# Optimization experiments

Measured on AMD Instinct MI355X. Metric: run time of the kernel, lower is better.

Reference implementation:

```python
import jax, jax.numpy as jnp
import numpy as np

L, D, DFF, H, B, S = 6, 1024, 4096, 16, 4, 512
DK = D // H
EPS = 1e-6


def setup_inputs() -> dict:
    key = jax.random.key(0)
    ks = jax.random.split(key, 20)
    sc = 0.02
    n = jax.random.normal
    return {
        "x": n(ks[0], (B, S, D), jnp.float32),
        "Wq": n(ks[1], (L, D, D)) * sc, "bq": jnp.zeros((L, D)),
        "Wk": n(ks[2], (L, D, D)) * sc, "bk": jnp.zeros((L, D)),
        "Wv": n(ks[3], (L, D, D)) * sc, "bv": jnp.zeros((L, D)),
        "Wo": n(ks[4], (L, D, D)) * sc, "bo": jnp.zeros((L, D)),
        "W1": n(ks[5], (L, D, DFF)) * sc, "b1": jnp.zeros((L, DFF)),
        "W2": n(ks[6], (L, DFF, D)) * sc, "b2": jnp.zeros((L, D)),
        "ln1_a": jnp.ones((L, D)), "ln1_b": jnp.zeros((L, D)),
        "ln2_a": jnp.ones((L, D)), "ln2_b": jnp.zeros((L, D)),
        "norm_a": jnp.ones((D,)), "norm_b": jnp.zeros((D,)),
    }


def _ln(x, a, b):
    # custom LayerNorm: uses sample std (ddof=1, like torch.std) and (std + eps)
    m = x.mean(-1, keepdims=True)
    s = jnp.std(x, axis=-1, ddof=1, keepdims=True)
    return a * (x - m) / (s + EPS) + b


def reference(x, Wq, bq, Wk, bk, Wv, bv, Wo, bo, W1, b1, W2, b2,
              ln1_a, ln1_b, ln2_a, ln2_b, norm_a, norm_b):
    inv = 1.0 / jnp.sqrt(jnp.float32(DK))
    for l in range(L):
        # --- self-attention sublayer (pre-norm, residual) ---
        h = _ln(x, ln1_a[l], ln1_b[l])
        q = (h @ Wq[l] + bq[l]).reshape(B, S, H, DK)
        k = (h @ Wk[l] + bk[l]).reshape(B, S, H, DK)
        v = (h @ Wv[l] + bv[l]).reshape(B, S, H, DK)
        scores = jnp.einsum('bqhd,bkhd->bhqk', q, k) * inv
        p = jax.nn.softmax(scores, axis=-1)
        o = jnp.einsum('bhqk,bkhd->bqhd', p, v).reshape(B, S, D)
        x = x + (o @ Wo[l] + bo[l])
        # --- feed-forward sublayer ---
        h = _ln(x, ln2_a[l], ln2_b[l])
        x = x + (jax.nn.relu(h @ W1[l] + b1[l]) @ W2[l] + b2[l])
    return _ln(x, norm_a, norm_b)
```

## Files before the change

### kernel.cpp

```cpp
#include <hip/hip_runtime.h>
#include <hip/hip_bf16.h>

typedef __hip_bfloat16 bf16;
typedef __bf16 bf16x8 __attribute__((ext_vector_type(8)));
typedef float f32x4 __attribute__((ext_vector_type(4)));

static constexpr int L_ = 6, D_ = 1024, DFF_ = 4096, H_ = 16, B_ = 4, S_ = 512, DK_ = 64;
static constexpr int N_ = B_ * S_;

#define GLOAD_LDS(gp, lp) __builtin_amdgcn_global_load_lds( \
    (const __attribute__((address_space(1))) void*)(gp),    \
    (__attribute__((address_space(3))) void*)(lp), 16, 0, 0)

__global__ void transpose_cast(const float* __restrict__ in, bf16* __restrict__ out,
                               int K, int M, long zin, long zout) {
    const float* ip = in + (size_t)blockIdx.z * zin;
    bf16* op = out + (size_t)blockIdx.z * zout;
    __shared__ float t[32][33];
    int m0 = blockIdx.x * 32, k0 = blockIdx.y * 32;
    int tx = threadIdx.x, ty = threadIdx.y;
    #pragma unroll
    for (int i = 0; i < 32; i += 8)
        t[ty + i][tx] = ip[(size_t)(k0 + ty + i) * M + m0 + tx];
    __syncthreads();
    #pragma unroll
    for (int i = 0; i < 32; i += 8)
        op[(size_t)(m0 + ty + i) * K + k0 + tx] = __float2bfloat16(t[tx][ty + i]);
}

__global__ void pack_qkv_bias(const float* __restrict__ bq, const float* __restrict__ bk,
                              const float* __restrict__ bv, float* __restrict__ out) {
    int t = blockIdx.x * 256 + threadIdx.x;
    int l = t / (3 * D_), c = t % (3 * D_);
    float v = c < D_ ? bq[l * D_ + c] : (c < 2 * D_ ? bk[l * D_ + c - D_] : bv[l * D_ + c - 2 * D_]);
    out[t] = v;
}

template <typename OutT>
__global__ __launch_bounds__(256) void ln_kernel(const float* __restrict__ x,
                                                 const float* __restrict__ ga,
                                                 const float* __restrict__ gb,
                                                 OutT* __restrict__ out) {
    int row = blockIdx.x;
    float4 v = ((const float4*)(x + (size_t)row * D_))[threadIdx.x];
    float s = v.x + v.y + v.z + v.w;
    float q = v.x * v.x + v.y * v.y + v.z * v.z + v.w * v.w;
    #pragma unroll
    for (int m = 1; m < 64; m <<= 1) { s += __shfl_xor(s, m, 64); q += __shfl_xor(q, m, 64); }
    __shared__ float ps[4], pq[4];
    int wid = threadIdx.x >> 6;
    if ((threadIdx.x & 63) == 0) { ps[wid] = s; pq[wid] = q; }
    __syncthreads();
    s = ps[0] + ps[1] + ps[2] + ps[3];
    q = pq[0] + pq[1] + pq[2] + pq[3];
    float mean = s * (1.0f / D_);
    float var = (q - (float)D_ * mean * mean) * (1.0f / (D_ - 1));
    var = var < 0.f ? 0.f : var;
    float rstd = 1.0f / (sqrtf(var) + 1e-6f);
    int c = threadIdx.x * 4;
    float xv[4] = {v.x, v.y, v.z, v.w};
    #pragma unroll
    for (int r = 0; r < 4; r++) {
        float o = ga[c + r] * (xv[r] - mean) * rstd + gb[c + r];
        if constexpr (__hip_internal::is_same<OutT, float>::value)
            out[(size_t)row * D_ + c + r] = o;
        else
            out[(size_t)row * D_ + c + r] = __float2bfloat16(o);
    }
}

template <int S, typename OutT>
__global__ __launch_bounds__(256) void reduce_ln(
    const bf16* __restrict__ parts, long sK, float* __restrict__ xf,
    const float* __restrict__ ga, const float* __restrict__ gb, OutT* __restrict__ out) {
    int row = blockIdx.x;
    float4 v = ((const float4*)(xf + (size_t)row * D_))[threadIdx.x];
    #pragma unroll
    for (int s = 0; s < S; s++) {
        ushort4 u = ((const ushort4*)(parts + (size_t)s * sK + (size_t)row * D_))[threadIdx.x];
        v.x += __uint_as_float((unsigned)u.x << 16);
        v.y += __uint_as_float((unsigned)u.y << 16);
        v.z += __uint_as_float((unsigned)u.z << 16);
        v.w += __uint_as_float((unsigned)u.w << 16);
    }
    ((float4*)(xf + (size_t)row * D_))[threadIdx.x] = v;
    float sum = v.x + v.y + v.z + v.w;
    float q = v.x * v.x + v.y * v.y + v.z * v.z + v.w * v.w;
    #pragma unroll
    for (int m = 1; m < 64; m <<= 1) { sum += __shfl_xor(sum, m, 64); q += __shfl_xor(q, m, 64); }
    __shared__ float ps[4], pq[4];
    int wid = threadIdx.x >> 6;
    if ((threadIdx.x & 63) == 0) { ps[wid] = sum; pq[wid] = q; }
    __syncthreads();
    sum = ps[0] + ps[1] + ps[2] + ps[3];
    q = pq[0] + pq[1] + pq[2] + pq[3];
    float mean = sum * (1.0f / D_);
    float var = (q - (float)D_ * mean * mean) * (1.0f / (D_ - 1));
    var = var < 0.f ? 0.f : var;
    float rstd = 1.0f / (sqrtf(var) + 1e-6f);
    int c = threadIdx.x * 4;
    float xv[4] = {v.x, v.y, v.z, v.w};
    #pragma unroll
    for (int r = 0; r < 4; r++) {
        float o = ga[c + r] * (xv[r] - mean) * rstd + gb[c + r];
        if constexpr (__hip_internal::is_same<OutT, float>::value)
            out[(size_t)row * D_ + c + r] = o;
        else
            out[(size_t)row * D_ + c + r] = __float2bfloat16(o);
    }
}

__device__ inline void swz_tiles(int& ntile, int& mtile) {
    unsigned o = blockIdx.y * gridDim.x + blockIdx.x;
    if ((gridDim.x & 7) == 0) {
        unsigned xcd = o & 7, j = o >> 3;
        unsigned cn = gridDim.x >> 3;
        ntile = xcd * cn + j / gridDim.y;
        mtile = j % gridDim.y;
    } else {
        ntile = o % gridDim.x;
        mtile = o / gridDim.x;
    }
}

enum { EPI_RELU = 0, EPI_PART = 1, EPI_QKV = 2 };

template <int EPI, int SPLITK = 1>
__global__ __launch_bounds__(256) void gemm4(
    const bf16* __restrict__ A, int lda,
    const bf16* __restrict__ Bt, int ldb,
    const float* __restrict__ bias,
    void* __restrict__ Cv, int ldc, long sK, int K,
    bf16* __restrict__ qb, bf16* __restrict__ kb, bf16* __restrict__ vT) {
    constexpr int BM = 128, BN = 64, BK = 64;
    constexpr int FM = 4, FN = 2;
    constexpr int IA = 4;
    constexpr int IB = 2;
    __shared__ __align__(16) bf16 As[BM * BK];
    __shared__ __align__(16) bf16 Bs[BN * BK];
    const int tid = threadIdx.x, wid = tid >> 6, lane = tid & 63;
    const int kz = (SPLITK > 1) ? blockIdx.z : 0;
    int ntile, mtile;
    swz_tiles(ntile, mtile);
    const int m0 = mtile * BM, n0 = ntile * BN;
    const int wm = (wid >> 1) * 64, wn = (wid & 1) * 32;
    const int fr = lane & 15, fg = lane >> 4;
    const int sr = lane >> 3;
    const int c8s = (lane & 7) ^ (sr & 7);
    const int Kc = K / SPLITK;
    const int kbeg = kz * Kc, kend = kbeg + Kc;

    f32x4 acc[FM][FN] = {};
    for (int k0 = kbeg; k0 < kend; k0 += BK) {
        __syncthreads();
        #pragma unroll
        for (int i = 0; i < IA; i++) {
            int inst = wid * IA + i;
            const bf16* gp = A + (size_t)(m0 + inst * 8 + sr) * lda + k0 + c8s * 8;
            GLOAD_LDS(gp, &As[inst * 512]);
        }
        #pragma unroll
        for (int i = 0; i < IB; i++) {
            int inst = wid * IB + i;
            const bf16* gp = Bt + (size_t)(n0 + inst * 8 + sr) * ldb + k0 + c8s * 8;
            GLOAD_LDS(gp, &Bs[inst * 512]);
        }
        __syncthreads();
        #pragma unroll
        for (int kk = 0; kk < 2; kk++) {
            const int cs = ((kk << 2) + fg) ^ (fr & 7);
            bf16x8 af[FM], bfr[FN];
            #pragma unroll
            for (int i = 0; i < FM; i++)
                af[i] = *(const bf16x8*)&As[(wm + i * 16 + fr) * BK + cs * 8];
            #pragma unroll
            for (int j = 0; j < FN; j++)
                bfr[j] = *(const bf16x8*)&Bs[(wn + j * 16 + fr) * BK + cs * 8];
            #pragma unroll
            for (int i = 0; i < FM; i++)
                #pragma unroll
                for (int j = 0; j < FN; j++)
                    acc[i][j] = __builtin_amdgcn_mfma_f32_16x16x32_bf16(af[i], bfr[j], acc[i][j], 0, 0, 0);
        }
    }
    #pragma unroll
    for (int i = 0; i < FM; i++) {
        #pragma unroll
        for (int j = 0; j < FN; j++) {
            int rr = m0 + wm + i * 16 + (lane >> 4) * 4;
            int cc = n0 + wn + j * 16 + (lane & 15);
            float bv = bias[cc];
            #pragma unroll
            for (int r = 0; r < 4; r++) {
                float v = acc[i][j][r];
                if constexpr (EPI == EPI_RELU) {
                    bf16* C = (bf16*)Cv;
                    float o = v + bv;
                    C[(size_t)(rr + r) * ldc + cc] = __float2bfloat16(o > 0.f ? o : 0.f);
                } else if constexpr (EPI == EPI_PART) {
                    bf16* C = (bf16*)Cv;
                    C[(size_t)kz * sK + (size_t)(rr + r) * ldc + cc] =
                        __float2bfloat16(v + (kz == 0 ? bv : 0.f));
                } else {
                    float o = v + bv;
                    if (cc < D_) {
                        qb[(size_t)(rr + r) * D_ + cc] = __float2bfloat16(o);
                    } else if (cc < 2 * D_) {
                        kb[(size_t)(rr + r) * D_ + cc - D_] = __float2bfloat16(o);
                    } else {
                        vT[((size_t)(rr >> 9) * D_ + cc - 2 * D_) * S_ + ((rr & 511) + r)] = __float2bfloat16(o);
                    }
                }
            }
        }
    }
}

__global__ __launch_bounds__(256) void flash_attn(
    const bf16* __restrict__ qb, const bf16* __restrict__ kb, const bf16* __restrict__ vT,
    bf16* __restrict__ ob) {
    __shared__ __align__(16) bf16 P[4][16 * 64];
    const int lane = threadIdx.x & 63, wid = threadIdx.x >> 6;
    const int b = blockIdx.y >> 4, h = blockIdx.y & 15;
    const int q0 = blockIdx.x * 64 + wid * 16;
    const int fr = lane & 15, fg = lane >> 4;
    bf16* Pw = &P[wid][0];

    const bf16* qrow = qb + ((size_t)(b * S_ + q0 + fr)) * D_ + h * DK_ + fg * 8;
    bf16x8 aq0 = *(const bf16x8*)(qrow);
    bf16x8 aq1 = *(const bf16x8*)(qrow + 32);
    const bf16* vbase = vT + ((size_t)(b * D_) + h * DK_ + fr) * S_ + fg * 8;

    f32x4 accO[4] = {};
    float mrow[4] = {-1e30f, -1e30f, -1e30f, -1e30f};
    float lrow[4] = {};

    #pragma unroll 2
    for (int kv0 = 0; kv0 < S_; kv0 += 64) {
        bf16x8 vv[2][4];
        #pragma unroll
        for (int ks = 0; ks < 2; ks++)
            #pragma unroll
            for (int j = 0; j < 4; j++)
                vv[ks][j] = *(const bf16x8*)(vbase + (size_t)j * 16 * S_ + kv0 + ks * 32);
        f32x4 s[4] = {};
        __builtin_amdgcn_s_setprio(1);
        #pragma unroll
        for (int j = 0; j < 4; j++) {
            const bf16* krow = kb + ((size_t)(b * S_ + kv0 + j * 16 + fr)) * D_ + h * DK_ + fg * 8;
            bf16x8 bk0 = *(const bf16x8*)(krow);
            bf16x8 bk1 = *(const bf16x8*)(krow + 32);
            s[j] = __builtin_amdgcn_mfma_f32_16x16x32_bf16(aq0, bk0, s[j], 0, 0, 0);
            s[j] = __builtin_amdgcn_mfma_f32_16x16x32_bf16(aq1, bk1, s[j], 0, 0, 0);
        }
        __builtin_amdgcn_s_setprio(0);
        float tmax[4], alpha[4], rs[4];
        #pragma unroll
        for (int r = 0; r < 4; r++) {
            #pragma unroll
            for (int j = 0; j < 4; j++) s[j][r] *= 0.125f;
            tmax[r] = fmaxf(fmaxf(s[0][r], s[1][r]), fmaxf(s[2][r], s[3][r]));
            #pragma unroll
            for (int m = 1; m < 16; m <<= 1) tmax[r] = fmaxf(tmax[r], __shfl_xor(tmax[r], m, 64));
            float mn = fmaxf(mrow[r], tmax[r]);
            alpha[r] = __expf(mrow[r] - mn);
            mrow[r] = mn;
            rs[r] = 0.f;
        }
        #pragma unroll
        for (int j = 0; j < 4; j++) {
            #pragma unroll
            for (int r = 0; r < 4; r++) {
                float p = __expf(s[j][r] - mrow[r]);
                rs[r] += p;
                int q = fg * 4 + r;
                int col = (j * 16 + fr) ^ ((q & 7) << 3);
                Pw[q * 64 + col] = __float2bfloat16(p);
            }
        }
        #pragma unroll
        for (int r = 0; r < 4; r++) {
            #pragma unroll
            for (int m = 1; m < 16; m <<= 1) rs[r] += __shfl_xor(rs[r], m, 64);
            lrow[r] = lrow[r] * alpha[r] + rs[r];
            #pragma unroll
            for (int j = 0; j < 4; j++) accO[j][r] *= alpha[r];
        }
        __builtin_amdgcn_s_setprio(1);
        #pragma unroll
        for (int ks = 0; ks < 2; ks++) {
            int kk = (ks * 32 + fg * 8) ^ ((fr & 7) << 3);
            bf16x8 ap = *(const bf16x8*)&Pw[fr * 64 + kk];
            #pragma unroll
            for (int j = 0; j < 4; j++)
                accO[j] = __builtin_amdgcn_mfma_f32_16x16x32_bf16(ap, vv[ks][j], accO[j], 0, 0, 0);
        }
        __builtin_amdgcn_s_setprio(0);
    }
    #pragma unroll
    for (int j = 0; j < 4; j++) {
        #pragma unroll
        for (int r = 0; r < 4; r++) {
            int q = q0 + fg * 4 + r;
            int d = h * DK_ + j * 16 + fr;
            ob[(size_t)(b * S_ + q) * D_ + d] = __float2bfloat16(accO[j][r] / lrow[r]);
        }
    }
}

extern "C" void kernel_launch(void* const* d_in, const int* in_sizes, int n_in,
                              void* d_out, int out_size, void* d_ws, size_t ws_size,
                              hipStream_t stream) {
    (void)in_sizes; (void)n_in; (void)out_size;
    const float* x    = (const float*)d_in[0];
    const float* Wq   = (const float*)d_in[1];
    const float* pbq  = (const float*)d_in[2];
    const float* Wk   = (const float*)d_in[3];
    const float* pbk  = (const float*)d_in[4];
    const float* Wv   = (const float*)d_in[5];
    const float* pbv  = (const float*)d_in[6];
    const float* Wo   = (const float*)d_in[7];
    const float* pbo  = (const float*)d_in[8];
    const float* W1   = (const float*)d_in[9];
    const float* pb1  = (const float*)d_in[10];
    const float* W2   = (const float*)d_in[11];
    const float* pb2  = (const float*)d_in[12];
    const float* l1a  = (const float*)d_in[13];
    const float* l1b  = (const float*)d_in[14];
    const float* l2a  = (const float*)d_in[15];
    const float* l2b  = (const float*)d_in[16];
    const float* nrma = (const float*)d_in[17];
    const float* nrmb = (const float*)d_in[18];

    char* ws = (char*)d_ws;
    size_t off = 0;
    auto alloc = [&](size_t bytes) { void* p = ws + off; off += (bytes + 255) & ~(size_t)255; return p; };
    float* xf  = (float*)alloc((size_t)N_ * D_ * 4);
    bf16* hbuf = (bf16*)alloc((size_t)N_ * D_ * 2);
    bf16* qbuf = (bf16*)alloc((size_t)N_ * D_ * 2);
    bf16* kbuf = (bf16*)alloc((size_t)N_ * D_ * 2);
    bf16* vT   = (bf16*)alloc((size_t)B_ * D_ * S_ * 2);
    bf16* obuf = (bf16*)alloc((size_t)N_ * D_ * 2);
    float* qkvb = (float*)alloc((size_t)L_ * 3 * D_ * 4);
    bf16* mid  = (bf16*)alloc((size_t)N_ * DFF_ * 2);
    bf16* wsP = (bf16*)alloc((size_t)4 * N_ * D_ * 2);
    const size_t szDD = (size_t)D_ * D_, szDF = (size_t)D_ * DFF_;
    const long sK = (long)N_ * D_;
    size_t wtFull = (3 * L_ * szDD + L_ * szDD + 2 * L_ * szDF) * 2;
    size_t wtLayer = (4 * szDD + 2 * szDF) * 2;
    bool full = (off + wtFull) <= ws_size;
    bf16* WT = (bf16*)alloc(full ? wtFull : wtLayer);

    pack_qkv_bias<<<L_ * 3 * D_ / 256, 256, 0, stream>>>(pbq, pbk, pbv, qkvb);

    bf16 *Wqkv0, *WoT0, *W1T0, *W2T0;
    dim3 tb(32, 8);
    if (full) {
        Wqkv0 = WT;
        WoT0  = WT + 3 * L_ * szDD;
        W1T0  = WoT0 + L_ * szDD;
        W2T0  = W1T0 + L_ * szDF;
        transpose_cast<<<dim3(D_ / 32, D_ / 32, L_), tb, 0, stream>>>(Wq, Wqkv0, D_, D_, szDD, 3 * szDD);
        transpose_cast<<<dim3(D_ / 32, D_ / 32, L_), tb, 0, stream>>>(Wk, Wqkv0 + szDD, D_, D_, szDD, 3 * szDD);
        transpose_cast<<<dim3(D_ / 32, D_ / 32, L_), tb, 0, stream>>>(Wv, Wqkv0 + 2 * szDD, D_, D_, szDD, 3 * szDD);
        transpose_cast<<<dim3(D_ / 32, D_ / 32, L_), tb, 0, stream>>>(Wo, WoT0, D_, D_, szDD, szDD);
        transpose_cast<<<dim3(DFF_ / 32, D_ / 32, L_), tb, 0, stream>>>(W1, W1T0, D_, DFF_, szDF, szDF);
        transpose_cast<<<dim3(D_ / 32, DFF_ / 32, L_), tb, 0, stream>>>(W2, W2T0, DFF_, D_, szDF, szDF);
    } else {
        Wqkv0 = WT; WoT0 = WT + 3 * szDD; W1T0 = WoT0 + szDD; W2T0 = W1T0 + szDF;
    }

    hipMemcpyAsync(xf, x, (size_t)N_ * D_ * 4, hipMemcpyDeviceToDevice, stream);
    ln_kernel<bf16><<<N_, 256, 0, stream>>>(xf, l1a, l1b, hbuf);

    for (int l = 0; l < L_; l++) {
        const bf16 *WqkvT, *WoT, *W1T, *W2T;
        if (full) {
            WqkvT = Wqkv0 + (size_t)l * 3 * szDD;
            WoT = WoT0 + l * szDD; W1T = W1T0 + l * szDF; W2T = W2T0 + l * szDF;
        } else {
            transpose_cast<<<dim3(D_ / 32, D_ / 32, 1), tb, 0, stream>>>(Wq + l * szDD, Wqkv0, D_, D_, 0, 0);
            transpose_cast<<<dim3(D_ / 32, D_ / 32, 1), tb, 0, stream>>>(Wk + l * szDD, Wqkv0 + szDD, D_, D_, 0, 0);
            transpose_cast<<<dim3(D_ / 32, D_ / 32, 1), tb, 0, stream>>>(Wv + l * szDD, Wqkv0 + 2 * szDD, D_, D_, 0, 0);
            transpose_cast<<<dim3(D_ / 32, D_ / 32, 1), tb, 0, stream>>>(Wo + l * szDD, WoT0, D_, D_, 0, 0);
            transpose_cast<<<dim3(DFF_ / 32, D_ / 32, 1), tb, 0, stream>>>(W1 + l * szDF, W1T0, D_, DFF_, 0, 0);
            transpose_cast<<<dim3(D_ / 32, DFF_ / 32, 1), tb, 0, stream>>>(W2 + l * szDF, W2T0, DFF_, D_, 0, 0);
            WqkvT = Wqkv0; WoT = WoT0; W1T = W1T0; W2T = W2T0;
        }

        gemm4<EPI_QKV><<<dim3(3 * D_ / 64, N_ / 128, 1), 256, 0, stream>>>(
            hbuf, D_, WqkvT, D_, qkvb + (size_t)l * 3 * D_, nullptr, 0, 0, D_, qbuf, kbuf, vT);
        flash_attn<<<dim3(S_ / 64, B_ * H_), 256, 0, stream>>>(qbuf, kbuf, vT, obuf);
        gemm4<EPI_PART, 2><<<dim3(D_ / 64, N_ / 128, 2), 256, 0, stream>>>(
            obuf, D_, WoT, D_, pbo + l * D_, wsP, D_, sK, D_, nullptr, nullptr, nullptr);
        reduce_ln<2, bf16><<<N_, 256, 0, stream>>>(wsP, sK, xf, l2a + l * D_, l2b + l * D_, hbuf);
        gemm4<EPI_RELU><<<dim3(DFF_ / 64, N_ / 128, 1), 256, 0, stream>>>(
            hbuf, D_, W1T, D_, pb1 + l * DFF_, mid, DFF_, 0, D_, nullptr, nullptr, nullptr);
        gemm4<EPI_PART, 4><<<dim3(D_ / 64, N_ / 128, 4), 256, 0, stream>>>(
            mid, DFF_, W2T, DFF_, pb2 + l * D_, wsP, D_, sK, DFF_, nullptr, nullptr, nullptr);
        if (l < L_ - 1)
            reduce_ln<4, bf16><<<N_, 256, 0, stream>>>(wsP, sK, xf, l1a + (l + 1) * D_, l1b + (l + 1) * D_, hbuf);
        else
            reduce_ln<4, float><<<N_, 256, 0, stream>>>(wsP, sK, xf, nrma, nrmb, (float*)d_out);
    }
}
```

Measured before the change: 1.025 ms.

## Split attention over KV halves with a separate softmax-combine kernel

The flash attention kernel now processes only half of the key/value sequence per block, doubling the grid from 512 to 1024 blocks. It writes unnormalized fp32 partial outputs plus per-row max and sum statistics. A new combine kernel merges the two halves with log-sum-exp rescaling and writes the bf16 attention output. This aims to raise occupancy across the GPU's compute units, at the cost of an extra launch and about 16MB of extra fp32 traffic per layer.

```diff
diff --git a/kernel.cpp b/kernel.cpp
--- a/kernel.cpp
+++ b/kernel.cpp
@@ -216,15 +216,18 @@
     }
 }
 
-__global__ __launch_bounds__(256) void flash_attn(
+template <int NSPL>
+__global__ __launch_bounds__(256) void flash_attn_part(
     const bf16* __restrict__ qb, const bf16* __restrict__ kb, const bf16* __restrict__ vT,
-    bf16* __restrict__ ob) {
+    float* __restrict__ oP, float* __restrict__ ml) {
     __shared__ __align__(16) bf16 P[4][16 * 64];
     const int lane = threadIdx.x & 63, wid = threadIdx.x >> 6;
     const int b = blockIdx.y >> 4, h = blockIdx.y & 15;
+    const int kz = blockIdx.z;
     const int q0 = blockIdx.x * 64 + wid * 16;
     const int fr = lane & 15, fg = lane >> 4;
     bf16* Pw = &P[wid][0];
+    constexpr int SC = S_ / NSPL;
 
     const bf16* qrow = qb + ((size_t)(b * S_ + q0 + fr)) * D_ + h * DK_ + fg * 8;
     bf16x8 aq0 = *(const bf16x8*)(qrow);
@@ -236,7 +239,7 @@
     float lrow[4] = {};
 
     #pragma unroll 2
-    for (int kv0 = 0; kv0 < S_; kv0 += 64) {
+    for (int kv0 = kz * SC; kv0 < (kz + 1) * SC; kv0 += 64) {
         bf16x8 vv[2][4];
         #pragma unroll
         for (int ks = 0; ks < 2; ks++)
@@ -303,9 +306,41 @@
         for (int r = 0; r < 4; r++) {
             int q = q0 + fg * 4 + r;
             int d = h * DK_ + j * 16 + fr;
-            ob[(size_t)(b * S_ + q) * D_ + d] = __float2bfloat16(accO[j][r] / lrow[r]);
-        }
-    }
+            oP[((size_t)kz * N_ + b * S_ + q) * D_ + d] = accO[j][r];
+        }
+    }
+    if (fr == 0) {
+        #pragma unroll
+        for (int r = 0; r < 4; r++) {
+            int q = q0 + fg * 4 + r;
+            size_t idx = (((size_t)kz * (B_ * H_) + blockIdx.y) * S_ + q) * 2;
+            ml[idx] = mrow[r];
+            ml[idx + 1] = lrow[r];
+        }
+    }
+}
+
+__global__ __launch_bounds__(256) void attn_combine(
+    const float* __restrict__ oP, const float* __restrict__ ml, bf16* __restrict__ ob) {
+    int row = blockIdx.x;
+    int b = row >> 9, q = row & 511;
+    int c = threadIdx.x;
+    int h = c >> 4;
+    int bh = b * H_ + h;
+    size_t i0 = (((size_t)0 * (B_ * H_) + bh) * S_ + q) * 2;
+    size_t i1 = (((size_t)1 * (B_ * H_) + bh) * S_ + q) * 2;
+    float m0 = ml[i0], l0 = ml[i0 + 1];
+    float m1 = ml[i1], l1 = ml[i1 + 1];
+    float m = fmaxf(m0, m1);
+    float s0 = __expf(m0 - m), s1 = __expf(m1 - m);
+    float inv = 1.0f / (l0 * s0 + l1 * s1);
+    float4 o0 = ((const float4*)(oP + (size_t)row * D_))[c];
+    float4 o1 = ((const float4*)(oP + ((size_t)N_ + row) * D_))[c];
+    bf16* op = ob + (size_t)row * D_ + c * 4;
+    op[0] = __float2bfloat16((o0.x * s0 + o1.x * s1) * inv);
+    op[1] = __float2bfloat16((o0.y * s0 + o1.y * s1) * inv);
+    op[2] = __float2bfloat16((o0.z * s0 + o1.z * s1) * inv);
+    op[3] = __float2bfloat16((o0.w * s0 + o1.w * s1) * inv);
 }
 
 extern "C" void kernel_launch(void* const* d_in, const int* in_sizes, int n_in,
@@ -344,6 +379,8 @@
     float* qkvb = (float*)alloc((size_t)L_ * 3 * D_ * 4);
     bf16* mid  = (bf16*)alloc((size_t)N_ * DFF_ * 2);
     bf16* wsP = (bf16*)alloc((size_t)4 * N_ * D_ * 2);
+    float* oP = (float*)alloc((size_t)2 * N_ * D_ * 4);
+    float* mlw = (float*)alloc((size_t)2 * B_ * H_ * S_ * 2 * 4);
     const size_t szDD = (size_t)D_ * D_, szDF = (size_t)D_ * DFF_;
     const long sK = (long)N_ * D_;
     size_t wtFull = (3 * L_ * szDD + L_ * szDD + 2 * L_ * szDF) * 2;
@@ -390,7 +427,8 @@
 
         gemm4<EPI_QKV><<<dim3(3 * D_ / 64, N_ / 128, 1), 256, 0, stream>>>(
             hbuf, D_, WqkvT, D_, qkvb + (size_t)l * 3 * D_, nullptr, 0, 0, D_, qbuf, kbuf, vT);
-        flash_attn<<<dim3(S_ / 64, B_ * H_), 256, 0, stream>>>(qbuf, kbuf, vT, obuf);
+        flash_attn_part<2><<<dim3(S_ / 64, B_ * H_, 2), 256, 0, stream>>>(qbuf, kbuf, vT, oP, mlw);
+        attn_combine<<<N_, 256, 0, stream>>>(oP, mlw, obuf);
         gemm4<EPI_PART, 2><<<dim3(D_ / 64, N_ / 128, 2), 256, 0, stream>>>(
             obuf, D_, WoT, D_, pbo + l * D_, wsP, D_, sK, D_, nullptr, nullptr, nullptr);
         reduce_ln<2, bf16><<<N_, 256, 0, stream>>>(wsP, sK, xf, l2a + l * D_, l2b + l * D_, hbuf);
```

Result: slower. 1.095 ms (+6.8%).
